# Optimization experiments

Measured on AMD Instinct MI355X. Metric: run time of the kernel, lower is better.

The kernel has to match this reference:

```python
import jax, jax.numpy as jnp
from jax import lax
import numpy as np

NUM_BINS = 4
GROUPS = 196
PS = 16  # patch_size
CH = 3 * GROUPS  # 588


def quick_gelu(x):
    return x * jax.nn.sigmoid(1.702 * x)


def avgpool3_exclude_pad(x):
    # AvgPool2d(kernel=3, stride=1, padding=1, count_include_pad=False)
    win = (1, 1, 3, 3)
    strides = (1, 1, 1, 1)
    pad = ((0, 0), (0, 0), (1, 1), (1, 1))
    s = lax.reduce_window(x, jnp.float32(0.0), lax.add, win, strides, pad)
    ones = jnp.ones((1, 1) + x.shape[-2:], x.dtype)
    cnt = lax.reduce_window(ones, jnp.float32(0.0), lax.add, win, strides, pad)
    return s / cnt


def setup_inputs() -> dict:
    key = jax.random.key(0)
    ks = jax.random.split(key, 6)
    B = 64
    x = jax.random.normal(ks[0], (B, 197, 768), jnp.float32)
    # adapter_conv: Conv2d(588,588,3,groups=196) -> OIHW weight [588,3,3,3]
    conv_w = jax.random.normal(ks[1], (CH, 3, 3, 3), jnp.float32) * (1.0 / np.sqrt(27.0))
    conv_b = jnp.zeros((CH,), jnp.float32)
    # HistogramLayer: bin_centers_conv.bias (learnable), bin_widths_conv.weight (learnable)
    centers = jax.random.normal(ks[2], (NUM_BINS * CH,), jnp.float32) * 0.1
    widths = jax.random.normal(ks[3], (NUM_BINS * CH,), jnp.float32) * 0.1 + 1.0
    # adapter_conv_down: Conv2d(2352,588,1,groups=196) -> per-group [3 out, 12 in]
    down_w = jax.random.normal(ks[4], (GROUPS, 3, 12), jnp.float32) * 0.1
    down_b = jax.random.normal(ks[5], (CH,), jnp.float32) * 0.1
    return dict(x=x, conv_w=conv_w, conv_b=conv_b, centers=centers,
                widths=widths, down_w=down_w, down_b=down_b)


def reference(x, conv_w, conv_b, centers, widths, down_w, down_b):
    B, N, C = x.shape  # (64, 197, 768)
    x_cls = x[:, :1, :]
    xp = x[:, 1:, :].reshape(B, (N - 1) * 3, PS, PS)  # (B, 588, 16, 16)

    # grouped 3x3 conv, groups=196 (3->3 per group)
    y = lax.conv_general_dilated(
        xp, conv_w, window_strides=(1, 1), padding=((1, 1), (1, 1)),
        dimension_numbers=('NCHW', 'OIHW', 'NCHW'), feature_group_count=GROUPS)
    y = y + conv_b[None, :, None, None]
    y = quick_gelu(y)

    # HistogramLayer: bin_centers (weight frozen at 1) -> abs; bin_widths (bias frozen at 1) -> relu
    h = jnp.abs(jnp.repeat(y, NUM_BINS, axis=1) + centers[None, :, None, None])  # (B, 2352, 16, 16)
    h = jax.nn.relu(widths[None, :, None, None] * h + 1.0)

    # constrain_bins: per-(channel-group of 4 bins) sum-normalize
    Bn, Cn, H, W = h.shape
    hr = h.reshape(Bn, Cn // NUM_BINS, NUM_BINS, H, W)
    h = (hr / (hr.sum(axis=2, keepdims=True) + 1e-5)).reshape(Bn, Cn, H, W)

    # normalize_count: AvgPool2d(3, stride=1, pad=1, count_include_pad=False)
    h = avgpool3_exclude_pad(h)
    h = quick_gelu(h)

    # adapter_conv_down: grouped 1x1 conv, 12 -> 3 per group of 196
    hg = h.reshape(B, GROUPS, 12, H, W)
    o = jnp.einsum('bgihw,goi->bgohw', hg, down_w) + down_b.reshape(1, GROUPS, 3, 1, 1)
    o = o.reshape(B, GROUPS, 768)  # (3*16*16 = 768 per patch token)

    return jnp.concatenate([x_cls, o], axis=1)  # (B, 197, 768)
```

## Files before the change

kernel.cpp:

```cpp
#include <hip/hip_runtime.h>

#define GROUPS 196

__device__ __forceinline__ float dppL(float v) {
    return __int_as_float(__builtin_amdgcn_update_dpp(
        __float_as_int(v), __float_as_int(v), 0x111, 0xF, 0xF, true));
}
__device__ __forceinline__ float dppR(float v) {
    return __int_as_float(__builtin_amdgcn_update_dpp(
        __float_as_int(v), __float_as_int(v), 0x101, 0xF, 0xF, true));
}
__device__ __forceinline__ float bperm(int addr, float v) {
    return __int_as_float(__builtin_amdgcn_ds_bpermute(addr, __float_as_int(v)));
}
__device__ __forceinline__ float qgelu(float v) {
    return v * __builtin_amdgcn_rcpf(1.0f + __expf(-1.702f * v));
}
__device__ __forceinline__ float qgelu01(float p) {
    return p * fmaf(p, fmaf(p, -0.11333f, 0.46195f), 0.49805f);
}

__global__ __launch_bounds__(256) void convpass_fused(
    const float* __restrict__ x,
    const float* __restrict__ conv_w,
    const float* __restrict__ conv_b,
    const float* __restrict__ centers,
    const float* __restrict__ widths,
    const float* __restrict__ down_w,
    const float* __restrict__ down_b,
    float* __restrict__ out)
{
    const int tid = threadIdx.x;
    const int l  = tid & 63;
    const int wv = tid >> 6;
    const int g  = blockIdx.x * 4 + wv;
    const int b  = blockIdx.y;
    const int q  = l >> 4;
    const int py = l & 15;
    const float mL = (q > 0) ? 1.f : 0.f;
    const float mR = (q < 3) ? 1.f : 0.f;
    const int aL = ((l - 16) & 63) << 2;
    const int aR = ((l + 16) & 63) << 2;

    const int sg = __builtin_amdgcn_readfirstlane(g);
    const float* cw  = conv_w  + sg * 81;
    const float* cen = centers + sg * 12;
    const float* wid = widths  + sg * 12;
    const float* dwp = down_w  + sg * 36;
    const float cb0 = conv_b[sg*3+0], cb1 = conv_b[sg*3+1], cb2 = conv_b[sg*3+2];
    const float db0 = down_b[sg*3+0], db1 = down_b[sg*3+1], db2 = down_b[sg*3+2];

    const int tok = b * 197 + g + 1;
    const float4* xin4 = (const float4*)x + tok * 192;
    const int fo = py * 4 + q;
    const float4 A0 = xin4[fo];
    const float4 A1 = xin4[64 + fo];
    const float4 A2 = xin4[128 + fo];

    float4 V[3][3];
    V[0][1] = A0; V[1][1] = A1; V[2][1] = A2;
    #pragma unroll
    for (int ic = 0; ic < 3; ++ic) {
        const float4 a = V[ic][1];
        V[ic][0] = make_float4(dppL(a.x), dppL(a.y), dppL(a.z), dppL(a.w));
        V[ic][2] = make_float4(dppR(a.x), dppR(a.y), dppR(a.z), dppR(a.w));
    }

    float L[3][3], R[3][3];
    #pragma unroll
    for (int ic = 0; ic < 3; ++ic) {
        const float eL = bperm(aL, V[ic][1].w) * mL;
        const float eR = bperm(aR, V[ic][1].x) * mR;
        L[ic][0] = dppL(eL); L[ic][1] = eL; L[ic][2] = dppR(eL);
        R[ic][0] = dppL(eR); R[ic][1] = eR; R[ic][2] = dppR(eR);
    }

    float acc[3][4];
    #pragma unroll
    for (int j = 0; j < 4; ++j) { acc[0][j] = cb0; acc[1][j] = cb1; acc[2][j] = cb2; }
    #pragma unroll
    for (int oc = 0; oc < 3; ++oc) {
        #pragma unroll
        for (int ic = 0; ic < 3; ++ic) {
            #pragma unroll
            for (int r = 0; r < 3; ++r) {
                const float w0 = cw[oc*27 + ic*9 + r*3 + 0];
                const float w1 = cw[oc*27 + ic*9 + r*3 + 1];
                const float w2 = cw[oc*27 + ic*9 + r*3 + 2];
                const float4 v = V[ic][r];
                acc[oc][0] = fmaf(L[ic][r], w0, fmaf(v.x, w1, fmaf(v.y, w2, acc[oc][0])));
                acc[oc][1] = fmaf(v.x,      w0, fmaf(v.y, w1, fmaf(v.z, w2, acc[oc][1])));
                acc[oc][2] = fmaf(v.y,      w0, fmaf(v.z, w1, fmaf(v.w, w2, acc[oc][2])));
                acc[oc][3] = fmaf(v.z,      w0, fmaf(v.w, w1, fmaf(R[ic][r], w2, acc[oc][3])));
            }
        }
    }

    float yv[3][4];
    #pragma unroll
    for (int oc = 0; oc < 3; ++oc)
        #pragma unroll
        for (int j = 0; j < 4; ++j)
            yv[oc][j] = qgelu(acc[oc][j]);

    const bool  vy2 = (py == 0) | (py == 15);
    const float rE = vy2 ? 0.25f     : (1.f/6.f);
    const float rM = vy2 ? (1.f/6.f) : (1.f/9.f);
    const float rc[4] = { (q == 0) ? rE : rM, rM, rM, (q == 3) ? rE : rM };

    float o[3][4];
    #pragma unroll
    for (int j = 0; j < 4; ++j) { o[0][j] = db0; o[1][j] = db1; o[2][j] = db2; }

    #pragma unroll
    for (int oc = 0; oc < 3; ++oc) {
        float hj[3][4];
        #pragma unroll
        for (int j = 0; j < 4; ++j) {
            const float y = yv[oc][j];
            const float t0 = fmaf(wid[oc*4+0], fabsf(y + cen[oc*4+0]), 1.0f);
            const float t1 = fmaf(wid[oc*4+1], fabsf(y + cen[oc*4+1]), 1.0f);
            const float t2 = fmaf(wid[oc*4+2], fabsf(y + cen[oc*4+2]), 1.0f);
            const float t3 = fmaf(wid[oc*4+3], fabsf(y + cen[oc*4+3]), 1.0f);
            const float inv = __builtin_amdgcn_rcpf((t0 + t1) + (t2 + t3));
            hj[0][j] = t0 * inv; hj[1][j] = t1 * inv; hj[2][j] = t2 * inv;
        }
        float rs[3][4];
        #pragma unroll
        for (int k = 0; k < 3; ++k) {
            const float lh = bperm(aL, hj[k][3]);
            const float rh = bperm(aR, hj[k][0]);
            const float s01 = hj[k][0] + hj[k][1];
            const float s23 = hj[k][2] + hj[k][3];
            rs[k][0] = fmaf(mL, lh, s01);
            rs[k][1] = s01 + hj[k][2];
            rs[k][2] = hj[k][1] + s23;
            rs[k][3] = fmaf(mR, rh, s23);
        }
        #pragma unroll
        for (int j = 0; j < 4; ++j) {
            const float v0 = rs[0][j] + dppL(rs[0][j]) + dppR(rs[0][j]);
            const float v1 = rs[1][j] + dppL(rs[1][j]) + dppR(rs[1][j]);
            const float v2 = rs[2][j] + dppL(rs[2][j]) + dppR(rs[2][j]);
            const float p0 = v0 * rc[j];
            const float p1 = v1 * rc[j];
            const float p2 = v2 * rc[j];
            const float p3 = 1.0f - p0 - p1 - p2;
            const float u0 = qgelu01(p0);
            const float u1 = qgelu01(p1);
            const float u2 = qgelu01(p2);
            const float u3 = qgelu01(p3);
            const int i = oc * 4;
            o[0][j] = fmaf(u0, dwp[i],    fmaf(u1, dwp[i+1],    fmaf(u2, dwp[i+2],    fmaf(u3, dwp[i+3],    o[0][j]))));
            o[1][j] = fmaf(u0, dwp[12+i], fmaf(u1, dwp[12+i+1], fmaf(u2, dwp[12+i+2], fmaf(u3, dwp[12+i+3], o[1][j]))));
            o[2][j] = fmaf(u0, dwp[24+i], fmaf(u1, dwp[24+i+1], fmaf(u2, dwp[24+i+2], fmaf(u3, dwp[24+i+3], o[2][j]))));
        }
    }

    float4* op4 = (float4*)out + tok * 192;
    op4[fo]       = make_float4(o[0][0], o[0][1], o[0][2], o[0][3]);
    op4[64 + fo]  = make_float4(o[1][0], o[1][1], o[1][2], o[1][3]);
    op4[128 + fo] = make_float4(o[2][0], o[2][1], o[2][2], o[2][3]);

    if (g == 0) {
        const float4* xc = (const float4*)x + b * 197 * 192;
        float4* oc4 = (float4*)out + b * 197 * 192;
        oc4[l]       = xc[l];
        oc4[64 + l]  = xc[64 + l];
        oc4[128 + l] = xc[128 + l];
    }
}

extern "C" void kernel_launch(void* const* d_in, const int* in_sizes, int n_in,
                              void* d_out, int out_size, void* d_ws, size_t ws_size,
                              hipStream_t stream) {
    const float* x       = (const float*)d_in[0];
    const float* conv_w  = (const float*)d_in[1];
    const float* conv_b  = (const float*)d_in[2];
    const float* centers = (const float*)d_in[3];
    const float* widths  = (const float*)d_in[4];
    const float* down_w  = (const float*)d_in[5];
    const float* down_b  = (const float*)d_in[6];
    float* out = (float*)d_out;

    const int B = in_sizes[0] / (197 * 768);

    dim3 grid(GROUPS / 4, B);
    convpass_fused<<<grid, 256, 0, stream>>>(x, conv_w, conv_b, centers, widths,
                                             down_w, down_b, out);
}
```

Baseline: 30.65 us.

## Compute histogram, pooling and down-projection in packed fp16 with dot2

The histogram bins, normalization, 3x3 average pooling, GELU polynomial and the grouped 1x1 down-projection now run on packed half2 values using packed fp16 math and v_dot2 accumulation into fp32. The fourth bin is computed explicitly rather than derived as one minus the other three. The goal is to halve VALU instruction count and the cross-lane permute/DPP traffic in the post-conv stage. The cost is reduced precision (fp16 with round-toward-zero packing), which may hurt accuracy, and extra pack/convert instructions.

```diff
diff --git a/kernel.cpp b/kernel.cpp
--- a/kernel.cpp
+++ b/kernel.cpp
@@ -2,22 +2,45 @@
 
 #define GROUPS 196
 
+typedef _Float16 half2v __attribute__((ext_vector_type(2)));
+
+__device__ __forceinline__ int dppLi(int v) {
+    return __builtin_amdgcn_update_dpp(v, v, 0x111, 0xF, 0xF, true);
+}
+__device__ __forceinline__ int dppRi(int v) {
+    return __builtin_amdgcn_update_dpp(v, v, 0x101, 0xF, 0xF, true);
+}
 __device__ __forceinline__ float dppL(float v) {
-    return __int_as_float(__builtin_amdgcn_update_dpp(
-        __float_as_int(v), __float_as_int(v), 0x111, 0xF, 0xF, true));
+    return __int_as_float(dppLi(__float_as_int(v)));
 }
 __device__ __forceinline__ float dppR(float v) {
-    return __int_as_float(__builtin_amdgcn_update_dpp(
-        __float_as_int(v), __float_as_int(v), 0x101, 0xF, 0xF, true));
+    return __int_as_float(dppRi(__float_as_int(v)));
+}
+__device__ __forceinline__ half2v dppL2(half2v v) {
+    return __builtin_bit_cast(half2v, dppLi(__builtin_bit_cast(int, v)));
+}
+__device__ __forceinline__ half2v dppR2(half2v v) {
+    return __builtin_bit_cast(half2v, dppRi(__builtin_bit_cast(int, v)));
 }
 __device__ __forceinline__ float bperm(int addr, float v) {
     return __int_as_float(__builtin_amdgcn_ds_bpermute(addr, __float_as_int(v)));
 }
+__device__ __forceinline__ half2v bperm2(int addr, half2v v) {
+    return __builtin_bit_cast(half2v,
+        __builtin_amdgcn_ds_bpermute(addr, __builtin_bit_cast(int, v)));
+}
+__device__ __forceinline__ half2v h2pack(float a, float b) {
+    return __builtin_bit_cast(half2v, __builtin_amdgcn_cvt_pkrtz(a, b));
+}
+__device__ __forceinline__ half2v h2abs(half2v a) {
+    const int i = __builtin_bit_cast(int, a) & 0x7FFF7FFF;
+    return __builtin_bit_cast(half2v, i);
+}
+__device__ __forceinline__ float fdot2(half2v a, half2v b, float c) {
+    return __builtin_amdgcn_fdot2(a, b, c, false);
+}
 __device__ __forceinline__ float qgelu(float v) {
     return v * __builtin_amdgcn_rcpf(1.0f + __expf(-1.702f * v));
-}
-__device__ __forceinline__ float qgelu01(float p) {
-    return p * fmaf(p, fmaf(p, -0.11333f, 0.46195f), 0.49805f);
 }
 
 __global__ __launch_bounds__(256) void convpass_fused(
@@ -47,8 +70,6 @@
     const float* cen = centers + sg * 12;
     const float* wid = widths  + sg * 12;
     const float* dwp = down_w  + sg * 36;
-    const float cb0 = conv_b[sg*3+0], cb1 = conv_b[sg*3+1], cb2 = conv_b[sg*3+2];
-    const float db0 = down_b[sg*3+0], db1 = down_b[sg*3+1], db2 = down_b[sg*3+2];
 
     const int tok = b * 197 + g + 1;
     const float4* xin4 = (const float4*)x + tok * 192;
@@ -65,7 +86,6 @@
         V[ic][0] = make_float4(dppL(a.x), dppL(a.y), dppL(a.z), dppL(a.w));
         V[ic][2] = make_float4(dppR(a.x), dppR(a.y), dppR(a.z), dppR(a.w));
     }
-
     float L[3][3], R[3][3];
     #pragma unroll
     for (int ic = 0; ic < 3; ++ic) {
@@ -76,8 +96,11 @@
     }
 
     float acc[3][4];
-    #pragma unroll
-    for (int j = 0; j < 4; ++j) { acc[0][j] = cb0; acc[1][j] = cb1; acc[2][j] = cb2; }
+    {
+        const float cb0 = conv_b[sg*3+0], cb1 = conv_b[sg*3+1], cb2 = conv_b[sg*3+2];
+        #pragma unroll
+        for (int j = 0; j < 4; ++j) { acc[0][j] = cb0; acc[1][j] = cb1; acc[2][j] = cb2; }
+    }
     #pragma unroll
     for (int oc = 0; oc < 3; ++oc) {
         #pragma unroll
@@ -96,64 +119,86 @@
         }
     }
 
-    float yv[3][4];
-    #pragma unroll
-    for (int oc = 0; oc < 3; ++oc)
-        #pragma unroll
-        for (int j = 0; j < 4; ++j)
-            yv[oc][j] = qgelu(acc[oc][j]);
+    half2v cen01[3], cen23[3], wid01[3], wid23[3];
+    half2v dw01[3][3], dw23[3][3];
+    #pragma unroll
+    for (int oc = 0; oc < 3; ++oc) {
+        cen01[oc] = h2pack(cen[oc*4+0], cen[oc*4+1]);
+        cen23[oc] = h2pack(cen[oc*4+2], cen[oc*4+3]);
+        wid01[oc] = h2pack(wid[oc*4+0], wid[oc*4+1]);
+        wid23[oc] = h2pack(wid[oc*4+2], wid[oc*4+3]);
+        #pragma unroll
+        for (int m = 0; m < 3; ++m) {
+            dw01[m][oc] = h2pack(dwp[m*12+oc*4+0], dwp[m*12+oc*4+1]);
+            dw23[m][oc] = h2pack(dwp[m*12+oc*4+2], dwp[m*12+oc*4+3]);
+        }
+    }
+    const half2v one2 = h2pack(1.f, 1.f);
+    const half2v mL2 = h2pack(mL, mL);
+    const half2v mR2 = h2pack(mR, mR);
+    const half2v C0 = h2pack(0.49805f, 0.49805f);
+    const half2v C1 = h2pack(0.46195f, 0.46195f);
+    const half2v C2 = h2pack(-0.11333f, -0.11333f);
 
     const bool  vy2 = (py == 0) | (py == 15);
     const float rE = vy2 ? 0.25f     : (1.f/6.f);
     const float rM = vy2 ? (1.f/6.f) : (1.f/9.f);
-    const float rc[4] = { (q == 0) ? rE : rM, rM, rM, (q == 3) ? rE : rM };
+    half2v rc2[4];
+    rc2[0] = h2pack((q == 0) ? rE : rM, (q == 0) ? rE : rM);
+    rc2[1] = h2pack(rM, rM);
+    rc2[2] = rc2[1];
+    rc2[3] = h2pack((q == 3) ? rE : rM, (q == 3) ? rE : rM);
 
     float o[3][4];
-    #pragma unroll
-    for (int j = 0; j < 4; ++j) { o[0][j] = db0; o[1][j] = db1; o[2][j] = db2; }
+    {
+        const float db0 = down_b[sg*3+0], db1 = down_b[sg*3+1], db2 = down_b[sg*3+2];
+        #pragma unroll
+        for (int j = 0; j < 4; ++j) { o[0][j] = db0; o[1][j] = db1; o[2][j] = db2; }
+    }
 
     #pragma unroll
     for (int oc = 0; oc < 3; ++oc) {
-        float hj[3][4];
+        half2v h01[4], h23[4];
         #pragma unroll
         for (int j = 0; j < 4; ++j) {
-            const float y = yv[oc][j];
-            const float t0 = fmaf(wid[oc*4+0], fabsf(y + cen[oc*4+0]), 1.0f);
-            const float t1 = fmaf(wid[oc*4+1], fabsf(y + cen[oc*4+1]), 1.0f);
-            const float t2 = fmaf(wid[oc*4+2], fabsf(y + cen[oc*4+2]), 1.0f);
-            const float t3 = fmaf(wid[oc*4+3], fabsf(y + cen[oc*4+3]), 1.0f);
-            const float inv = __builtin_amdgcn_rcpf((t0 + t1) + (t2 + t3));
-            hj[0][j] = t0 * inv; hj[1][j] = t1 * inv; hj[2][j] = t2 * inv;
-        }
-        float rs[3][4];
-        #pragma unroll
-        for (int k = 0; k < 3; ++k) {
-            const float lh = bperm(aL, hj[k][3]);
-            const float rh = bperm(aR, hj[k][0]);
-            const float s01 = hj[k][0] + hj[k][1];
-            const float s23 = hj[k][2] + hj[k][3];
-            rs[k][0] = fmaf(mL, lh, s01);
-            rs[k][1] = s01 + hj[k][2];
-            rs[k][2] = hj[k][1] + s23;
-            rs[k][3] = fmaf(mR, rh, s23);
+            const float y = qgelu(acc[oc][j]);
+            const half2v y2 = h2pack(y, y);
+            const half2v t01 = wid01[oc] * h2abs(y2 + cen01[oc]) + one2;
+            const half2v t23 = wid23[oc] * h2abs(y2 + cen23[oc]) + one2;
+            const float sum = fdot2(t01, one2, fdot2(t23, one2, 0.f));
+            const float inv = __builtin_amdgcn_rcpf(sum);
+            const half2v inv2 = h2pack(inv, inv);
+            h01[j] = t01 * inv2;
+            h23[j] = t23 * inv2;
+        }
+        half2v rs01[4], rs23[4];
+        {
+            const half2v lh01 = bperm2(aL, h01[3]);
+            const half2v lh23 = bperm2(aL, h23[3]);
+            const half2v rh01 = bperm2(aR, h01[0]);
+            const half2v rh23 = bperm2(aR, h23[0]);
+            const half2v sa01 = h01[0] + h01[1], sb01 = h01[2] + h01[3];
+            const half2v sa23 = h23[0] + h23[1], sb23 = h23[2] + h23[3];
+            rs01[0] = mL2 * lh01 + sa01;
+            rs01[1] = sa01 + h01[2];
+            rs01[2] = h01[1] + sb01;
+            rs01[3] = mR2 * rh01 + sb01;
+            rs23[0] = mL2 * lh23 + sa23;
+            rs23[1] = sa23 + h23[2];
+            rs23[2] = h23[1] + sb23;
+            rs23[3] = mR2 * rh23 + sb23;
         }
         #pragma unroll
         for (int j = 0; j < 4; ++j) {
-            const float v0 = rs[0][j] + dppL(rs[0][j]) + dppR(rs[0][j]);
-            const float v1 = rs[1][j] + dppL(rs[1][j]) + dppR(rs[1][j]);
-            const float v2 = rs[2][j] + dppL(rs[2][j]) + dppR(rs[2][j]);
-            const float p0 = v0 * rc[j];
-            const float p1 = v1 * rc[j];
-            const float p2 = v2 * rc[j];
-            const float p3 = 1.0f - p0 - p1 - p2;
-            const float u0 = qgelu01(p0);
-            const float u1 = qgelu01(p1);
-            const float u2 = qgelu01(p2);
-            const float u3 = qgelu01(p3);
-            const int i = oc * 4;
-            o[0][j] = fmaf(u0, dwp[i],    fmaf(u1, dwp[i+1],    fmaf(u2, dwp[i+2],    fmaf(u3, dwp[i+3],    o[0][j]))));
-            o[1][j] = fmaf(u0, dwp[12+i], fmaf(u1, dwp[12+i+1], fmaf(u2, dwp[12+i+2], fmaf(u3, dwp[12+i+3], o[1][j]))));
-            o[2][j] = fmaf(u0, dwp[24+i], fmaf(u1, dwp[24+i+1], fmaf(u2, dwp[24+i+2], fmaf(u3, dwp[24+i+3], o[2][j]))));
+            const half2v v01 = rs01[j] + dppL2(rs01[j]) + dppR2(rs01[j]);
+            const half2v v23 = rs23[j] + dppL2(rs23[j]) + dppR2(rs23[j]);
+            const half2v p01 = v01 * rc2[j];
+            const half2v p23 = v23 * rc2[j];
+            const half2v u01 = p01 * (C0 + p01 * (C1 + p01 * C2));
+            const half2v u23 = p23 * (C0 + p23 * (C1 + p23 * C2));
+            o[0][j] = fdot2(u01, dw01[0][oc], fdot2(u23, dw23[0][oc], o[0][j]));
+            o[1][j] = fdot2(u01, dw01[1][oc], fdot2(u23, dw23[1][oc], o[1][j]));
+            o[2][j] = fdot2(u01, dw01[2][oc], fdot2(u23, dw23[2][oc], o[2][j]));
         }
     }
 
```

After: 30.13 us. No clear change (-1.7%).
